# Kernel optimization log

Measured on AMD Instinct MI355X. Metric: run time of the kernel, lower is better.

The kernel has to match this reference:

```python
import jax, jax.numpy as jnp
import numpy as np

B, S, D, H = 2, 2048, 1024, 16
DK = D // H


def setup_inputs() -> dict:
    key = jax.random.key(0)
    ks = jax.random.split(key, 11)
    s = 1.0 / np.sqrt(D)
    inp = {
        "q": jax.random.normal(ks[0], (B, S, D), jnp.float32),
        "k": jax.random.normal(ks[1], (B, S, D), jnp.float32),
        "v": jax.random.normal(ks[2], (B, S, D), jnp.float32),
        "mask": jnp.tril(jnp.ones((S, S), jnp.int32))[None, None],  # [1,1,S,S] causal
        "Wq": jax.random.normal(ks[3], (D, D), jnp.float32) * s,
        "bq": jnp.zeros((D,), jnp.float32),
        "Wk": jax.random.normal(ks[4], (D, D), jnp.float32) * s,
        "bk": jnp.zeros((D,), jnp.float32),
        "Wv": jax.random.normal(ks[5], (D, D), jnp.float32) * s,
        "bv": jnp.zeros((D,), jnp.float32),
        "Wo": jax.random.normal(ks[6], (D, D), jnp.float32) * s,
        "bo": jnp.zeros((D,), jnp.float32),
    }
    return inp


def reference(q, k, v, mask, Wq, bq, Wk, bk, Wv, bv, Wo, bo):
    # projections -> [B, H, S, DK]
    def split_heads(x):
        return x.reshape(B, S, H, DK).transpose(0, 2, 1, 3)

    Q = split_heads(q @ Wq + bq)
    K = split_heads(k @ Wk + bk)
    V = split_heads(v @ Wv + bv)

    scores = jnp.einsum("bhqd,bhkd->bhqk", Q, K) / jnp.sqrt(jnp.float32(DK))
    scores = jnp.where(mask == 0, jnp.float32(-1e9), scores)
    # source applies dropout(p=0.0) here -> identity
    attn = jax.nn.softmax(scores, axis=-1)  # [B,H,S,S]
    x = jnp.einsum("bhqk,bhkd->bhqd", attn, V)
    x = x.transpose(0, 2, 1, 3).reshape(B, S, D)
    return x @ Wo + bo
```

## Files before the change

kernel.cpp:

```cpp
#include <hip/hip_runtime.h>
#include <hip/hip_bf16.h>
#include <stdint.h>

#define Bb 2
#define Ss 2048
#define Dd 1024
#define Hh 16
#define DKk 64

#define QSCALE 0.180336878f

typedef __attribute__((ext_vector_type(8))) short s8v;
typedef __attribute__((ext_vector_type(4))) short s4v;
typedef __attribute__((ext_vector_type(4))) float f4v;
typedef __attribute__((ext_vector_type(16))) float f16v;

#if __has_builtin(__builtin_amdgcn_exp2f)
#define EXP2(x) __builtin_amdgcn_exp2f(x)
#else
#define EXP2(x) __expf((x)*0.69314718f)
#endif

__device__ __forceinline__ unsigned short f2bf(float f) {
    __hip_bfloat16 h = __float2bfloat16(f);
    union { __hip_bfloat16 h; unsigned short u; } c; c.h = h;
    return c.u;
}

__device__ __forceinline__ unsigned pack_bf2(float lo, float hi) {
    __hip_bfloat162 h = __float22bfloat162_rn(float2{lo, hi});
    union { __hip_bfloat162 h; unsigned u; } c; c.h = h;
    return c.u;
}

__device__ __forceinline__ void gload16(const void* g, void* l) {
    __builtin_amdgcn_global_load_lds((__attribute__((address_space(1))) void*)g,
                                     (__attribute__((address_space(3))) void*)l, 16, 0, 0);
}

__global__ void __launch_bounds__(256) prep_x(const float* __restrict__ q,
                                              const float* __restrict__ k,
                                              const float* __restrict__ v,
                                              unsigned short* __restrict__ xq,
                                              unsigned short* __restrict__ xk,
                                              unsigned short* __restrict__ xv) {
    const int z = blockIdx.z;
    const float* s = (z == 0) ? q : ((z == 1) ? k : v);
    unsigned short* d = (z == 0) ? xq : ((z == 1) ? xk : xv);
    long i = ((long)blockIdx.x * blockDim.x + threadIdx.x) * 8;
    f4v a = *(const f4v*)(s + i);
    f4v b = *(const f4v*)(s + i + 4);
    union { unsigned u[4]; s8v v; } o;
    o.u[0] = pack_bf2(a[0], a[1]);
    o.u[1] = pack_bf2(a[2], a[3]);
    o.u[2] = pack_bf2(b[0], b[1]);
    o.u[3] = pack_bf2(b[2], b[3]);
    *(s8v*)(void*)(d + i) = o.v;
}

__global__ void __launch_bounds__(256) prep_w(const float* __restrict__ Wq,
                                              const float* __restrict__ Wk,
                                              const float* __restrict__ Wv,
                                              const float* __restrict__ Wo,
                                              unsigned short* __restrict__ o0,
                                              unsigned short* __restrict__ o1,
                                              unsigned short* __restrict__ o2,
                                              unsigned short* __restrict__ o3) {
    __shared__ float t[64][65];
    const int z = blockIdx.z;
    const float* W = (z == 0) ? Wq : ((z == 1) ? Wk : ((z == 2) ? Wv : Wo));
    unsigned short* O = (z == 0) ? o0 : ((z == 1) ? o1 : ((z == 2) ? o2 : o3));
    const int n0 = (blockIdx.x & 15) * 64;
    const int k0 = (blockIdx.x >> 4) * 64;
    const int c = threadIdx.x & 63;
    const int r4 = threadIdx.x >> 6;
#pragma unroll
    for (int i = 0; i < 16; i++) {
        int r = i * 4 + r4;
        t[r][c] = W[(long)(k0 + r) * Dd + n0 + c];
    }
    __syncthreads();
#pragma unroll
    for (int i = 0; i < 16; i++) {
        int r = i * 4 + r4;
        O[(long)(n0 + r) * Dd + k0 + c] = f2bf(t[c][r]);
    }
}

template <int MODE>
__device__ __forceinline__ void gemm_body(const unsigned short* __restrict__ A,
                                          const unsigned short* __restrict__ Bt,
                                          const float* __restrict__ bias,
                                          void* __restrict__ out, float oscale,
                                          unsigned short* smem) {
    unsigned short* As = smem;
    unsigned short* Bs = smem + 128 * 64;
    const int tid = threadIdx.x;
    const int l = tid & 63;
    const int w = tid >> 6;
    const int wr = w >> 1, wc = w & 1;
    const int lr = l & 15, lg = l >> 4;
    const int m0 = blockIdx.y * 128;
    const int n0 = blockIdx.x * 128;

    f4v acc[4][4];
#pragma unroll
    for (int m = 0; m < 4; m++)
#pragma unroll
        for (int n = 0; n < 4; n++) acc[m][n] = (f4v){0.f, 0.f, 0.f, 0.f};

    const int srow = tid >> 3;
    const int sg = (tid & 7) ^ (srow & 7);
    char* lbaseA = (char*)As + w * 1024;
    char* lbaseB = (char*)Bs + w * 1024;

    for (int t = 0; t < 16; t++) {
        const int k0 = t * 64;
#pragma unroll
        for (int i = 0; i < 4; i++) {
            int rowA = i * 32 + srow;
            gload16((const char*)A + ((long)(m0 + rowA) * 1024 + k0) * 2 + sg * 16,
                    lbaseA + i * 4096);
            gload16((const char*)Bt + ((long)(n0 + rowA) * 1024 + k0) * 2 + sg * 16,
                    lbaseB + i * 4096);
        }
        __syncthreads();
#pragma unroll
        for (int kk = 0; kk < 2; kk++) {
            s8v af[4], bfr[4];
#pragma unroll
            for (int m = 0; m < 4; m++) {
                int row = wr * 64 + m * 16 + lr;
                int gc = (kk * 4 + lg) ^ (row & 7);
                af[m] = *(const s8v*)((const char*)As + row * 128 + gc * 16);
            }
#pragma unroll
            for (int n = 0; n < 4; n++) {
                int row = wc * 64 + n * 16 + lr;
                int gc = (kk * 4 + lg) ^ (row & 7);
                bfr[n] = *(const s8v*)((const char*)Bs + row * 128 + gc * 16);
            }
#pragma unroll
            for (int m = 0; m < 4; m++)
#pragma unroll
                for (int n = 0; n < 4; n++)
                    acc[m][n] = __builtin_amdgcn_mfma_f32_16x16x32_bf16(af[m], bfr[n],
                                                                        acc[m][n], 0, 0, 0);
        }
        __syncthreads();
    }

#pragma unroll
    for (int n = 0; n < 4; n++) {
        int col = n0 + wc * 64 + n * 16 + lr;
        float bv = bias[col];
#pragma unroll
        for (int m = 0; m < 4; m++) {
#pragma unroll
            for (int r = 0; r < 4; r++) {
                int row = m0 + wr * 64 + m * 16 + lg * 4 + r;
                float val = acc[m][n][r] + bv;
                if (MODE == 0) {
                    int b = row >> 11, s2 = row & 2047, h = col >> 6, d = col & 63;
                    ((unsigned short*)out)[(((b * Hh + h) * Ss + s2) << 6) + d] =
                        f2bf(val * oscale);
                } else if (MODE == 1) {
                    int b = row >> 11, s2 = row & 2047, h = col >> 6, d = col & 63;
                    ((unsigned short*)out)[((b * Hh + h) * DKk + d) * Ss + s2] = f2bf(val);
                } else {
                    ((float*)out)[(long)row * Dd + col] = val;
                }
            }
        }
    }
}

__global__ void __launch_bounds__(256) qkv_gemm(const unsigned short* __restrict__ xq,
                                                const unsigned short* __restrict__ xk,
                                                const unsigned short* __restrict__ xv,
                                                const unsigned short* __restrict__ Wqt,
                                                const unsigned short* __restrict__ Wkt,
                                                const unsigned short* __restrict__ Wvt,
                                                const float* __restrict__ bq,
                                                const float* __restrict__ bk,
                                                const float* __restrict__ bv,
                                                unsigned short* __restrict__ Qh,
                                                unsigned short* __restrict__ Kh,
                                                unsigned short* __restrict__ Vt) {
    __shared__ unsigned short smem[128 * 64 * 2];
    const int z = blockIdx.z;
    if (z == 0)
        gemm_body<0>(xq, Wqt, bq, Qh, QSCALE, smem);
    else if (z == 1)
        gemm_body<0>(xk, Wkt, bk, Kh, 1.f, smem);
    else
        gemm_body<1>(xv, Wvt, bv, Vt, 1.f, smem);
}

__global__ void __launch_bounds__(256) out_gemm(const unsigned short* __restrict__ x,
                                                const unsigned short* __restrict__ Wot,
                                                const float* __restrict__ bo,
                                                float* __restrict__ out) {
    __shared__ unsigned short smem[128 * 64 * 2];
    gemm_body<2>(x, Wot, bo, out, 1.f, smem);
}

__global__ void __launch_bounds__(256) attn_kernel(const unsigned short* __restrict__ Qh,
                                                   const unsigned short* __restrict__ Kh,
                                                   const unsigned short* __restrict__ Vt,
                                                   unsigned short* __restrict__ xatt) {
    __shared__ float plds[2][64][34];
    const int tid = threadIdx.x;
    const int w = tid >> 6, l = tid & 63;
    const int lq = l & 31;
    const int hi = l >> 5;
    const int bh = blockIdx.x & 31;
    const int tile = 63 - (blockIdx.x >> 5);
    const int q0 = tile * 32;
    const int b = bh >> 4, h = bh & 15;
    const unsigned short* Qp = Qh + bh * Ss * DKk;
    const unsigned short* Kp = Kh + bh * Ss * DKk;
    const unsigned short* Vp = Vt + bh * DKk * Ss;

    s8v qf[4];
#pragma unroll
    for (int kk = 0; kk < 4; kk++)
        qf[kk] = *(const s8v*)(Qp + (q0 + lq) * 64 + kk * 16 + hi * 8);

    f16v oT0, oT1;
#pragma unroll
    for (int r = 0; r < 16; r++) { oT0[r] = 0.f; oT1[r] = 0.f; }
    float mx = -1e30f, sm = 0.f;
    const int nkb = tile + 1;

    for (int kb = w; kb < nkb; kb += 4) {
        const int k0 = kb * 32;
        s8v kf[4], vf0[2], vf1[2];
#pragma unroll
        for (int kk = 0; kk < 4; kk++)
            kf[kk] = *(const s8v*)(Kp + (k0 + lq) * 64 + kk * 16 + hi * 8);
#pragma unroll
        for (int kk = 0; kk < 2; kk++) {
            vf0[kk] = *(const s8v*)(Vp + lq * Ss + k0 + kk * 16 + hi * 8);
            vf1[kk] = *(const s8v*)(Vp + (32 + lq) * Ss + k0 + kk * 16 + hi * 8);
        }

        f16v S;
#pragma unroll
        for (int r = 0; r < 16; r++) S[r] = 0.f;
#pragma unroll
        for (int kk = 0; kk < 4; kk++)
            S = __builtin_amdgcn_mfma_f32_32x32x16_bf16(kf[kk], qf[kk], S, 0, 0, 0);

        const bool diag = (kb == nkb - 1);
        float e[16];
        float pmax = -1e30f;
#pragma unroll
        for (int r = 0; r < 16; r++) {
            float v = S[r];
            if (diag) {
                int kv = k0 + (r & 3) + 8 * (r >> 2) + 4 * hi;
                if (kv > q0 + lq) v = -1e30f;
            }
            e[r] = v;
            pmax = fmaxf(pmax, v);
        }
        pmax = fmaxf(pmax, __shfl_xor(pmax, 32));

        if (!__all(pmax - mx <= 8.f)) {
            float mn = fmaxf(mx, pmax);
            float sc = EXP2(mx - mn);
            mx = mn;
            sm *= sc;
#pragma unroll
            for (int r = 0; r < 16; r++) { oT0[r] *= sc; oT1[r] *= sc; }
        }
        float rs = 0.f;
#pragma unroll
        for (int r = 0; r < 16; r++) {
            e[r] = EXP2(e[r] - mx);
            rs += e[r];
        }
        rs += __shfl_xor(rs, 32);
        sm += rs;

        unsigned pk[8], sw[8];
#pragma unroll
        for (int i = 0; i < 8; i++)
            pk[i] = pack_bf2(e[2 * i], e[2 * i + 1]);
#pragma unroll
        for (int i = 0; i < 8; i++)
            sw[i] = (unsigned)__shfl_xor((int)pk[i], 32);

        union { unsigned u[4]; s8v v; } p0, p1;
        p0.u[0] = hi ? sw[2] : pk[0];
        p0.u[1] = hi ? sw[3] : pk[1];
        p0.u[2] = hi ? pk[2] : sw[0];
        p0.u[3] = hi ? pk[3] : sw[1];
        p1.u[0] = hi ? sw[6] : pk[4];
        p1.u[1] = hi ? sw[7] : pk[5];
        p1.u[2] = hi ? pk[6] : sw[4];
        p1.u[3] = hi ? pk[7] : sw[5];

        oT0 = __builtin_amdgcn_mfma_f32_32x32x16_bf16(vf0[0], p0.v, oT0, 0, 0, 0);
        oT0 = __builtin_amdgcn_mfma_f32_32x32x16_bf16(vf0[1], p1.v, oT0, 0, 0, 0);
        oT1 = __builtin_amdgcn_mfma_f32_32x32x16_bf16(vf1[0], p0.v, oT1, 0, 0, 0);
        oT1 = __builtin_amdgcn_mfma_f32_32x32x16_bf16(vf1[1], p1.v, oT1, 0, 0, 0);
    }

    if (w >= 2) {
        float* p = plds[w - 2][l];
        p[0] = mx; p[1] = sm;
#pragma unroll
        for (int r = 0; r < 16; r++) { p[2 + r] = oT0[r]; p[18 + r] = oT1[r]; }
    }
    __syncthreads();
    if (w < 2) {
        const float* p = plds[w][l];
        float m2 = p[0], s2 = p[1];
        float M = fmaxf(mx, m2);
        float a = EXP2(mx - M), bb = EXP2(m2 - M);
        sm = sm * a + s2 * bb;
#pragma unroll
        for (int r = 0; r < 16; r++) {
            oT0[r] = oT0[r] * a + p[2 + r] * bb;
            oT1[r] = oT1[r] * a + p[18 + r] * bb;
        }
        mx = M;
    }
    __syncthreads();
    if (w == 1) {
        float* p = plds[0][l];
        p[0] = mx; p[1] = sm;
#pragma unroll
        for (int r = 0; r < 16; r++) { p[2 + r] = oT0[r]; p[18 + r] = oT1[r]; }
    }
    __syncthreads();
    if (w != 0) return;
    {
        const float* p = plds[0][l];
        float m2 = p[0], s2 = p[1];
        float M = fmaxf(mx, m2);
        float a = EXP2(mx - M), bb = EXP2(m2 - M);
        sm = sm * a + s2 * bb;
#pragma unroll
        for (int r = 0; r < 16; r++) {
            oT0[r] = oT0[r] * a + p[2 + r] * bb;
            oT1[r] = oT1[r] * a + p[18 + r] * bb;
        }
    }

    const float inv = 1.f / sm;
    const int q = q0 + lq;
    unsigned short* orow = xatt + (long)(b * Ss + q) * Dd + h * 64;
#pragma unroll
    for (int g = 0; g < 4; g++) {
        union { unsigned u[2]; s4v v; } v0, v1;
        v0.u[0] = pack_bf2(oT0[g * 4 + 0] * inv, oT0[g * 4 + 1] * inv);
        v0.u[1] = pack_bf2(oT0[g * 4 + 2] * inv, oT0[g * 4 + 3] * inv);
        v1.u[0] = pack_bf2(oT1[g * 4 + 0] * inv, oT1[g * 4 + 1] * inv);
        v1.u[1] = pack_bf2(oT1[g * 4 + 2] * inv, oT1[g * 4 + 3] * inv);
        int d = 8 * g + 4 * hi;
        *(s4v*)(orow + d) = v0.v;
        *(s4v*)(orow + 32 + d) = v1.v;
    }
}

extern "C" void kernel_launch(void* const* d_in, const int* in_sizes, int n_in,
                              void* d_out, int out_size, void* d_ws, size_t ws_size,
                              hipStream_t stream) {
    const float* q  = (const float*)d_in[0];
    const float* k  = (const float*)d_in[1];
    const float* v  = (const float*)d_in[2];
    const float* Wq = (const float*)d_in[4];
    const float* bq = (const float*)d_in[5];
    const float* Wk = (const float*)d_in[6];
    const float* bk = (const float*)d_in[7];
    const float* Wv = (const float*)d_in[8];
    const float* bv = (const float*)d_in[9];
    const float* Wo = (const float*)d_in[10];
    const float* bo = (const float*)d_in[11];
    float* out = (float*)d_out;

    char* ws = (char*)d_ws;
    unsigned short* xq  = (unsigned short*)(ws + 0);
    unsigned short* xk  = (unsigned short*)(ws + 8388608);
    unsigned short* xv  = (unsigned short*)(ws + 16777216);
    unsigned short* Wqt = (unsigned short*)(ws + 25165824);
    unsigned short* Wkt = (unsigned short*)(ws + 27262976);
    unsigned short* Wvt = (unsigned short*)(ws + 29360128);
    unsigned short* Wot = (unsigned short*)(ws + 31457280);
    unsigned short* Qh  = (unsigned short*)(ws + 33554432);
    unsigned short* Kh  = (unsigned short*)(ws + 41943040);
    unsigned short* Vtp = (unsigned short*)(ws + 50331648);
    unsigned short* xat = (unsigned short*)(ws + 58720256);

    prep_x<<<dim3(2048, 1, 3), 256, 0, stream>>>(q, k, v, xq, xk, xv);
    prep_w<<<dim3(256, 1, 4), 256, 0, stream>>>(Wq, Wk, Wv, Wo, Wqt, Wkt, Wvt, Wot);
    qkv_gemm<<<dim3(8, 32, 3), 256, 0, stream>>>(xq, xk, xv, Wqt, Wkt, Wvt,
                                                 bq, bk, bv, Qh, Kh, Vtp);
    attn_kernel<<<dim3(2048), 256, 0, stream>>>(Qh, Kh, Vtp, xat);
    out_gemm<<<dim3(8, 32), 256, 0, stream>>>(xat, Wot, bo, out);
}
```

Baseline: 159.1 us.

## Stage K/V chunks through swizzled LDS in attention kernel

The attention kernel now loads each 128-key chunk of K and V cooperatively into XOR-swizzled shared memory using the gload16 path. Each wave then reads its 32-key block from LDS instead of issuing strided per-wave global loads. The row max and row sum reductions are also reorganised into trees. The change adds two block barriers per chunk with no double buffering, so load latency is not overlapped with compute. It also relies on the existing gload16 helper and aliases the merge buffer onto the same LDS.

```diff
diff --git a/kernel.cpp b/kernel.cpp
--- a/kernel.cpp
+++ b/kernel.cpp
@@ -209,7 +209,9 @@
                                                    const unsigned short* __restrict__ Kh,
                                                    const unsigned short* __restrict__ Vt,
                                                    unsigned short* __restrict__ xatt) {
-    __shared__ float plds[2][64][34];
+    __shared__ __align__(16) char ldsbuf[32768];
+    unsigned short* Ks = (unsigned short*)ldsbuf;
+    unsigned short* Vs = (unsigned short*)(ldsbuf + 16384);
     const int tid = threadIdx.x;
     const int w = tid >> 6, l = tid & 63;
     const int lq = l & 31;
@@ -232,82 +234,115 @@
     for (int r = 0; r < 16; r++) { oT0[r] = 0.f; oT1[r] = 0.f; }
     float mx = -1e30f, sm = 0.f;
     const int nkb = tile + 1;
-
-    for (int kb = w; kb < nkb; kb += 4) {
-        const int k0 = kb * 32;
-        s8v kf[4], vf0[2], vf1[2];
-#pragma unroll
-        for (int kk = 0; kk < 4; kk++)
-            kf[kk] = *(const s8v*)(Kp + (k0 + lq) * 64 + kk * 16 + hi * 8);
-#pragma unroll
-        for (int kk = 0; kk < 2; kk++) {
-            vf0[kk] = *(const s8v*)(Vp + lq * Ss + k0 + kk * 16 + hi * 8);
-            vf1[kk] = *(const s8v*)(Vp + (32 + lq) * Ss + k0 + kk * 16 + hi * 8);
-        }
-
-        f16v S;
-#pragma unroll
-        for (int r = 0; r < 16; r++) S[r] = 0.f;
-#pragma unroll
-        for (int kk = 0; kk < 4; kk++)
-            S = __builtin_amdgcn_mfma_f32_32x32x16_bf16(kf[kk], qf[kk], S, 0, 0, 0);
-
-        const bool diag = (kb == nkb - 1);
-        float e[16];
-        float pmax = -1e30f;
-#pragma unroll
-        for (int r = 0; r < 16; r++) {
-            float v = S[r];
-            if (diag) {
-                int kv = k0 + (r & 3) + 8 * (r >> 2) + 4 * hi;
-                if (kv > q0 + lq) v = -1e30f;
-            }
-            e[r] = v;
-            pmax = fmaxf(pmax, v);
-        }
-        pmax = fmaxf(pmax, __shfl_xor(pmax, 32));
-
-        if (!__all(pmax - mx <= 8.f)) {
-            float mn = fmaxf(mx, pmax);
-            float sc = EXP2(mx - mn);
-            mx = mn;
-            sm *= sc;
-#pragma unroll
-            for (int r = 0; r < 16; r++) { oT0[r] *= sc; oT1[r] *= sc; }
-        }
-        float rs = 0.f;
-#pragma unroll
-        for (int r = 0; r < 16; r++) {
-            e[r] = EXP2(e[r] - mx);
-            rs += e[r];
-        }
-        rs += __shfl_xor(rs, 32);
-        sm += rs;
-
-        unsigned pk[8], sw[8];
-#pragma unroll
-        for (int i = 0; i < 8; i++)
-            pk[i] = pack_bf2(e[2 * i], e[2 * i + 1]);
-#pragma unroll
-        for (int i = 0; i < 8; i++)
-            sw[i] = (unsigned)__shfl_xor((int)pk[i], 32);
-
-        union { unsigned u[4]; s8v v; } p0, p1;
-        p0.u[0] = hi ? sw[2] : pk[0];
-        p0.u[1] = hi ? sw[3] : pk[1];
-        p0.u[2] = hi ? pk[2] : sw[0];
-        p0.u[3] = hi ? pk[3] : sw[1];
-        p1.u[0] = hi ? sw[6] : pk[4];
-        p1.u[1] = hi ? sw[7] : pk[5];
-        p1.u[2] = hi ? pk[6] : sw[4];
-        p1.u[3] = hi ? pk[7] : sw[5];
-
-        oT0 = __builtin_amdgcn_mfma_f32_32x32x16_bf16(vf0[0], p0.v, oT0, 0, 0, 0);
-        oT0 = __builtin_amdgcn_mfma_f32_32x32x16_bf16(vf0[1], p1.v, oT0, 0, 0, 0);
-        oT1 = __builtin_amdgcn_mfma_f32_32x32x16_bf16(vf1[0], p0.v, oT1, 0, 0, 0);
-        oT1 = __builtin_amdgcn_mfma_f32_32x32x16_bf16(vf1[1], p1.v, oT1, 0, 0, 0);
-    }
-
+    const int nch = (nkb + 3) >> 2;
+
+    for (int ch = 0; ch < nch; ch++) {
+        const int kv0 = ch * 128;
+#pragma unroll
+        for (int i = 0; i < 4; i++) {
+            const int G0 = i * 256 + w * 64;
+            int G = G0 + l;
+            int row = G >> 3, gd = G & 7;
+            int gs = gd ^ (row & 7);
+            gload16(Kp + (kv0 + row) * 64 + gs * 8, (char*)Ks + G0 * 16);
+        }
+#pragma unroll
+        for (int i = 0; i < 4; i++) {
+            const int G0 = i * 256 + w * 64;
+            int G = G0 + l;
+            int row = G >> 4, gd = G & 15;
+            int gs = gd ^ (row & 15);
+            gload16(Vp + (long)row * Ss + kv0 + gs * 8, (char*)Vs + G0 * 16);
+        }
+        __syncthreads();
+
+        const int kb = ch * 4 + w;
+        if (kb < nkb) {
+            const int k0 = kb * 32;
+            s8v kf[4];
+#pragma unroll
+            for (int kk = 0; kk < 4; kk++) {
+                int row = w * 32 + lq;
+                int g = (2 * kk + hi) ^ (row & 7);
+                kf[kk] = *(const s8v*)((const char*)Ks + (row * 8 + g) * 16);
+            }
+            s8v vf0[2], vf1[2];
+#pragma unroll
+            for (int kk = 0; kk < 2; kk++) {
+                int g0 = 4 * w + 2 * kk + hi;
+                vf0[kk] = *(const s8v*)((const char*)Vs + (lq * 16 + (g0 ^ (lq & 15))) * 16);
+                vf1[kk] =
+                    *(const s8v*)((const char*)Vs + ((32 + lq) * 16 + (g0 ^ (lq & 15))) * 16);
+            }
+
+            f16v S;
+#pragma unroll
+            for (int r = 0; r < 16; r++) S[r] = 0.f;
+#pragma unroll
+            for (int kk = 0; kk < 4; kk++)
+                S = __builtin_amdgcn_mfma_f32_32x32x16_bf16(kf[kk], qf[kk], S, 0, 0, 0);
+
+            const bool diag = (kb == nkb - 1);
+            float e[16];
+#pragma unroll
+            for (int r = 0; r < 16; r++) {
+                float v = S[r];
+                if (diag) {
+                    int kv = k0 + (r & 3) + 8 * (r >> 2) + 4 * hi;
+                    if (kv > q0 + lq) v = -1e30f;
+                }
+                e[r] = v;
+            }
+            float m8[8];
+#pragma unroll
+            for (int i = 0; i < 8; i++) m8[i] = fmaxf(e[i], e[i + 8]);
+#pragma unroll
+            for (int i = 0; i < 4; i++) m8[i] = fmaxf(m8[i], m8[i + 4]);
+            float pmax = fmaxf(fmaxf(m8[0], m8[1]), fmaxf(m8[2], m8[3]));
+            pmax = fmaxf(pmax, __shfl_xor(pmax, 32));
+
+            if (!__all(pmax - mx <= 8.f)) {
+                float mn = fmaxf(mx, pmax);
+                float sc = EXP2(mx - mn);
+                mx = mn;
+                sm *= sc;
+#pragma unroll
+                for (int r = 0; r < 16; r++) { oT0[r] *= sc; oT1[r] *= sc; }
+            }
+#pragma unroll
+            for (int r = 0; r < 16; r++) e[r] = EXP2(e[r] - mx);
+            float s8s[8];
+#pragma unroll
+            for (int i = 0; i < 8; i++) s8s[i] = e[i] + e[i + 8];
+#pragma unroll
+            for (int i = 0; i < 4; i++) s8s[i] = s8s[i] + s8s[i + 4];
+            float rs = (s8s[0] + s8s[1]) + (s8s[2] + s8s[3]);
+            sm += rs + __shfl_xor(rs, 32);
+
+            unsigned pk[8], sw[8];
+#pragma unroll
+            for (int i = 0; i < 8; i++) pk[i] = pack_bf2(e[2 * i], e[2 * i + 1]);
+#pragma unroll
+            for (int i = 0; i < 8; i++) sw[i] = (unsigned)__shfl_xor((int)pk[i], 32);
+            union { unsigned u[4]; s8v v; } p0, p1;
+            p0.u[0] = hi ? sw[2] : pk[0];
+            p0.u[1] = hi ? sw[3] : pk[1];
+            p0.u[2] = hi ? pk[2] : sw[0];
+            p0.u[3] = hi ? pk[3] : sw[1];
+            p1.u[0] = hi ? sw[6] : pk[4];
+            p1.u[1] = hi ? sw[7] : pk[5];
+            p1.u[2] = hi ? pk[6] : sw[4];
+            p1.u[3] = hi ? pk[7] : sw[5];
+
+            oT0 = __builtin_amdgcn_mfma_f32_32x32x16_bf16(vf0[0], p0.v, oT0, 0, 0, 0);
+            oT0 = __builtin_amdgcn_mfma_f32_32x32x16_bf16(vf0[1], p1.v, oT0, 0, 0, 0);
+            oT1 = __builtin_amdgcn_mfma_f32_32x32x16_bf16(vf1[0], p0.v, oT1, 0, 0, 0);
+            oT1 = __builtin_amdgcn_mfma_f32_32x32x16_bf16(vf1[1], p1.v, oT1, 0, 0, 0);
+        }
+        __syncthreads();
+    }
+
+    float(*plds)[64][34] = (float(*)[64][34])ldsbuf;
     if (w >= 2) {
         float* p = plds[w - 2][l];
         p[0] = mx; p[1] = sm;
```

Result: faster. 149.2 us (-6.2%).
